# Kernel tuning notes

Hardware: AMD Instinct MI355X
Metric: run time of the kernel (lower is better)

The kernel has to match this reference:

```python
import jax, jax.numpy as jnp
import numpy as np

KSIZE = 21
SCALE = 4

def _conv1x1(h, w, b):
    # h: (B, Ci, H, W), w: (Co, Ci), b: (Co,)
    return jnp.einsum('oi,bihw->bohw', w, h) + b[None, :, None, None]

def setup_inputs() -> dict:
    key = jax.random.key(0)
    ks = jax.random.split(key, 8)
    B, C, H, W = 16, 3, 256, 256
    in_nc, nf, nb, K2 = 64, 64, 8, KSIZE * KSIZE
    Hl, Wl = H // SCALE, W // SCALE
    wscale = 0.1
    return {
        'x': jax.random.normal(ks[0], (B, C, H, W), jnp.float32),
        'z': jax.random.normal(ks[1], (B, in_nc, Hl, Wl), jnp.float32),
        'w_in': wscale * jax.random.normal(ks[2], (nf, in_nc), jnp.float32),
        'b_in': jnp.zeros((nf,), jnp.float32),
        'res_w1': wscale * jax.random.normal(ks[3], (nb, nf, nf), jnp.float32),
        'res_b1': jnp.zeros((nb, nf), jnp.float32),
        'res_w2': wscale * jax.random.normal(ks[4], (nb, nf, nf), jnp.float32),
        'res_b2': jnp.zeros((nb, nf), jnp.float32),
        'w_out': wscale * jax.random.normal(ks[5], (K2, nf), jnp.float32),
        'b_out': jnp.zeros((K2,), jnp.float32),
    }

def reference(x, z, w_in, b_in, res_w1, res_b1, res_w2, res_b2, w_out, b_out):
    B, C, H, W = x.shape
    Hl, Wl = z.shape[2], z.shape[3]
    K2 = KSIZE * KSIZE
    pad = KSIZE // 2

    # --- kernel prediction trunk (all 1x1 convs) ---
    h = _conv1x1(z, w_in, b_in)
    for i in range(res_w1.shape[0]):  # fixed n_layers loop
        r = _conv1x1(h, res_w1[i], res_b1[i])
        r = _conv1x1(jax.nn.relu(r), res_w2[i], res_b2[i])
        h = h + r
    logits = _conv1x1(h, w_out, b_out)            # (B, K2, Hl, Wl)
    kernel = jax.nn.softmax(logits, axis=1)       # softmax over kernel taps

    # --- reflection pad + unfold (im2col) with stride=scale ---
    xp = jnp.pad(x, ((0, 0), (0, 0), (pad, pad), (pad, pad)), mode='reflect')
    xr = xp.reshape(B * C, 1, H + 2 * pad, W + 2 * pad)
    patches = jax.lax.conv_general_dilated_patches(
        xr, filter_shape=(KSIZE, KSIZE), window_strides=(SCALE, SCALE),
        padding='VALID', dimension_numbers=('NCHW', 'OIHW', 'NCHW'))
    patches = patches.reshape(B, C, K2, Hl, Wl)   # (B, C, K2, Hl, Wl)

    # --- per-pixel spatially-varying kernel apply ---
    out = (patches * kernel[:, None]).sum(axis=2)  # (B, C, Hl, Wl)
    return out, kernel
```

## Files before the change

### kernel.cpp

```cpp
#include <hip/hip_runtime.h>
#include <math.h>

#define KS 21
#define K2 441
#define NB 8
#define PPI 4096
#define NPIX 65536
#define STR 72
#define XW 276
#define BPX 128
#define NTH 512
#define XROWS 25

typedef unsigned short u16;
typedef unsigned int u32;
typedef short short8v __attribute__((ext_vector_type(8)));
typedef float f32x4 __attribute__((ext_vector_type(4)));
typedef float f32x16 __attribute__((ext_vector_type(16)));

#define WOUT_OFF 69632
#define BOUT_BYTE 196608

#define LDS_HBUF  0
#define LDS_XS    18432
#define LDS_SBUF  59840
#define LDS_OBUF  60864
#define LDS_TOTAL 63936

__device__ __forceinline__ u16 f2bf(float x)
{
    union { float f; u32 u; } c; c.f = x;
    u32 r = c.u + 0x7FFF + ((c.u >> 16) & 1);
    return (u16)(r >> 16);
}
__device__ __forceinline__ float bflo(u32 w)
{ union { u32 u; float f; } c; c.u = w << 16; return c.f; }
__device__ __forceinline__ float bfhi(u32 w)
{ union { u32 u; float f; } c; c.u = w & 0xffff0000u; return c.f; }
__device__ __forceinline__ float u16f(u16 h)
{ union { u32 u; float f; } c; c.u = ((u32)h) << 16; return c.f; }

__device__ __forceinline__ int xcd_swz(int i)
{
    return ((i & 7) << 6) | (i >> 3);
}

__global__ void prep_kernel(const float* __restrict__ w_in,
                            const float* __restrict__ rw1,
                            const float* __restrict__ rw2,
                            const float* __restrict__ w_out,
                            const float* __restrict__ b_out,
                            u16* __restrict__ wsu, float* __restrict__ bout)
{
    int idx = blockIdx.x * 256 + threadIdx.x;
    if (idx < 69632) {
        int u = idx & 4095;
        int j = u & 7, lane = (u >> 3) & 63, frag = (u >> 9) & 7;
        int kk = frag >> 2, nt = frag & 3, layer = idx >> 12;
        int i = kk * 32 + (lane >> 4) * 8 + j;
        int o = nt * 16 + (lane & 15);
        const float* src;
        if (layer == 0) src = w_in;
        else if (layer & 1) src = rw1 + ((layer - 1) >> 1) * 4096;
        else src = rw2 + ((layer - 2) >> 1) * 4096;
        wsu[idx] = f2bf(src[o * 64 + i]);
    } else if (idx < 69632 + 28672) {
        int u = idx - 69632;
        int j = u & 7, lane = (u >> 3) & 63, t6 = u >> 9;
        int t = t6 % 14, kk = t6 / 14;
        int tap = t * 32 + (lane & 31);
        int i = kk * 16 + (lane >> 5) * 8 + j;
        wsu[idx] = f2bf((tap < K2) ? w_out[tap * 64 + i] : 0.f);
    } else if (idx < 69632 + 28672 + 448) {
        int tap = idx - (69632 + 28672);
        bout[tap] = (tap < K2) ? b_out[tap] : -100.f;
    }
}

__device__ __forceinline__ int reflect256(int v)
{
    v = (v < 0) ? -v : v;
    return (v > 255) ? (510 - v) : v;
}

template <int MODE>
__device__ __forceinline__ void do_layer(u16* hb, const u16* __restrict__ wb,
                                         const float* __restrict__ bias,
                                         float* hreg, int aoff, int wbase,
                                         int c, int g, int lane)
{
    short8v a0 = *(const short8v*)(hb + aoff);
    short8v a1 = *(const short8v*)(hb + aoff + 32);
#pragma unroll
    for (int nt = 0; nt < 4; ++nt) {
        f32x4 acc = {};
        short8v b0 = *(const short8v*)(wb + ((nt)     * 64 + lane) * 8);
        short8v b1 = *(const short8v*)(wb + ((4 + nt) * 64 + lane) * 8);
        acc = __builtin_amdgcn_mfma_f32_16x16x32_bf16(a0, b0, acc, 0, 0, 0);
        acc = __builtin_amdgcn_mfma_f32_16x16x32_bf16(a1, b1, acc, 0, 0, 0);
        const float bv = bias[nt * 16 + c];
#pragma unroll
        for (int r = 0; r < 4; ++r) {
            float v = acc[r] + bv;
            if (MODE == 1) v = fmaxf(v, 0.f);
            if (MODE == 2) { v += hreg[nt * 4 + r]; hreg[nt * 4 + r] = v; }
            if (MODE == 0) hreg[nt * 4 + r] = v;
            hb[(wbase + g * 4 + r) * STR + nt * 16 + c] = f2bf(v);
        }
    }
}

__launch_bounds__(NTH, 4)
__global__ void trunk_kernel(const float* __restrict__ z,
                             const float* __restrict__ x,
                             const float* __restrict__ b_in,
                             const float* __restrict__ rb1,
                             const float* __restrict__ rb2,
                             const u16* __restrict__ wsu,
                             const float* __restrict__ bout,
                             float* __restrict__ out,
                             float* __restrict__ kout)
{
    extern __shared__ __align__(16) char smem[];
    u16*   hbuf = (u16*)(smem + LDS_HBUF);
    u16*   xs   = (u16*)(smem + LDS_XS);
    float* sbuf = (float*)(smem + LDS_SBUF);
    float* obuf = (float*)(smem + LDS_OBUF);

    const int tid = threadIdx.x, lane = tid & 63, wave = tid >> 6;
    const int pix0 = xcd_swz(blockIdx.x) * BPX;
    const int b = pix0 >> 12, rem0 = pix0 & 4095;
    const int hl0 = rem0 >> 6;

    {
        const int p = tid & 127, i0 = (tid >> 7) * 16;
        const float* zp = z + ((size_t)b * 64 + i0) * PPI + rem0 + p;
        u32* dst = (u32*)hbuf + p * (STR / 2) + i0 / 2;
#pragma unroll
        for (int i = 0; i < 16; i += 2) {
            float v0 = zp[(size_t)i * PPI];
            float v1 = zp[(size_t)(i + 1) * PPI];
            dst[i / 2] = (u32)f2bf(v0) | ((u32)f2bf(v1) << 16);
        }
    }
    for (int u = tid; u < XROWS * 3 * XW; u += NTH) {
        int t = u / XW;
        int j = u - t * XW;
        int rr = t / 3, cch = t - rr * 3;
        int row = reflect256(hl0 * 4 + rr - 10);
        int xcol = reflect256(j - 10);
        xs[u] = f2bf(x[(((size_t)b * 3 + cch) * 256 + row) * 256 + xcol]);
    }
    __syncthreads();

    const int c16 = lane & 15, g4 = lane >> 4;
    const int wbase = wave * 16;
    const int aoff = (wbase + c16) * STR + g4 * 8;
    float hreg[16];

    do_layer<0>(hbuf, wsu, b_in, hreg, aoff, wbase, c16, g4, lane);
#pragma unroll 1
    for (int l = 0; l < NB; ++l) {
        do_layer<1>(hbuf, wsu + (size_t)(1 + 2 * l) * 4096, rb1 + l * 64,
                    hreg, aoff, wbase, c16, g4, lane);
        do_layer<2>(hbuf, wsu + (size_t)(2 + 2 * l) * 4096, rb2 + l * 64,
                    hreg, aoff, wbase, c16, g4, lane);
    }
    __syncthreads();

    const int c32 = lane & 31, hi2 = lane >> 5;
    const int wavepx = (wave >> 1) * 32;
    const int tbase = (wave & 1) * 7;

    short8v bh[4];
#pragma unroll
    for (int kk = 0; kk < 4; ++kk)
        bh[kk] = *(const short8v*)(hbuf + (wavepx + c32) * STR + kk * 16 + hi2 * 8);

    float ssum = 0.f;
    u32 epack[56];
    const u16* wob = wsu + WOUT_OFF;
#pragma unroll
    for (int ti = 0; ti < 7; ++ti) {
        const int t = tbase + ti;
        f32x16 acc = {};
#pragma unroll
        for (int kk = 0; kk < 4; ++kk) {
            short8v aw = *(const short8v*)(wob + ((kk * 14 + t) * 64 + lane) * 8);
            acc = __builtin_amdgcn_mfma_f32_32x32x16_bf16(aw, bh[kk], acc, 0, 0, 0);
        }
#pragma unroll
        for (int rr = 0; rr < 8; ++rr) {
            const int r0 = 2 * rr;
            const int tap0 = t * 32 + (r0 & 3) + 8 * (r0 >> 2) + 4 * hi2;
            float e0 = __expf(acc[r0] + bout[tap0]);
            float e1 = __expf(acc[r0 + 1] + bout[tap0 + 1]);
            ssum += e0 + e1;
            epack[ti * 8 + rr] = (u32)f2bf(e0) | ((u32)f2bf(e1) << 16);
        }
    }
    ssum += __shfl_xor(ssum, 32);
    if (lane < 32) sbuf[wave * 32 + lane] = ssum;
    __syncthreads();
    const float inv_s = 1.f / (ssum + sbuf[(wave ^ 1) * 32 + c32]);

    const int pxl = wavepx + c32;
    const int wl = pxl & 63, hlr = pxl >> 6;
    const int xcb = wl * 4;
    float* kbase = kout + (size_t)b * K2 * PPI + rem0 + pxl;
    float oacc0 = 0.f, oacc1 = 0.f, oacc2 = 0.f;

#pragma unroll
    for (int ti = 0; ti < 7; ++ti) {
        const int t = tbase + ti;
        int tap = t * 32 + 4 * hi2;
        int ky = tap / KS;
        int kx = tap - ky * KS;
#pragma unroll
        for (int rr = 0; rr < 8; ++rr) {
            const u32 ep = epack[ti * 8 + rr];
            float p0 = bflo(ep) * inv_s;
            float p1 = bfhi(ep) * inv_s;
            if (tap < K2) {
                kbase[(size_t)tap * PPI] = p0;
                const u16* xp = xs + ((hlr * 4 + ky) * 3) * XW + xcb + kx;
                oacc0 = fmaf(p0, u16f(xp[0]), oacc0);
                oacc1 = fmaf(p0, u16f(xp[XW]), oacc1);
                oacc2 = fmaf(p0, u16f(xp[2 * XW]), oacc2);
            }
            tap += 1; kx += 1; if (kx >= KS) { kx -= KS; ky += 1; }
            if (tap < K2) {
                kbase[(size_t)tap * PPI] = p1;
                const u16* xp = xs + ((hlr * 4 + ky) * 3) * XW + xcb + kx;
                oacc0 = fmaf(p1, u16f(xp[0]), oacc0);
                oacc1 = fmaf(p1, u16f(xp[XW]), oacc1);
                oacc2 = fmaf(p1, u16f(xp[2 * XW]), oacc2);
            }
            const int d = (rr & 1) ? 5 : 1;
            tap += d; kx += d; if (kx >= KS) { kx -= KS; ky += 1; }
        }
    }

    oacc0 += __shfl_xor(oacc0, 32);
    oacc1 += __shfl_xor(oacc1, 32);
    oacc2 += __shfl_xor(oacc2, 32);
    if (lane < 32) {
        obuf[(wave * 3 + 0) * 32 + lane] = oacc0;
        obuf[(wave * 3 + 1) * 32 + lane] = oacc1;
        obuf[(wave * 3 + 2) * 32 + lane] = oacc2;
    }
    __syncthreads();
    if ((wave & 1) == 0 && lane < 32) {
        const int o = rem0 + wavepx + lane;
#pragma unroll
        for (int cch = 0; cch < 3; ++cch) {
            float v = obuf[(wave * 3 + cch) * 32 + lane] +
                      obuf[((wave + 1) * 3 + cch) * 32 + lane];
            out[((size_t)b * 3 + cch) * PPI + o] = v;
        }
    }
}

extern "C" void kernel_launch(void* const* d_in, const int* in_sizes, int n_in,
                              void* d_out, int out_size, void* d_ws, size_t ws_size,
                              hipStream_t stream)
{
    const float* x     = (const float*)d_in[0];
    const float* z     = (const float*)d_in[1];
    const float* w_in  = (const float*)d_in[2];
    const float* b_in  = (const float*)d_in[3];
    const float* rw1   = (const float*)d_in[4];
    const float* rb1   = (const float*)d_in[5];
    const float* rw2   = (const float*)d_in[6];
    const float* rb2   = (const float*)d_in[7];
    const float* w_out = (const float*)d_in[8];
    const float* b_out = (const float*)d_in[9];

    float* out  = (float*)d_out;
    float* kout = out + (size_t)16 * 3 * PPI;
    u16*   wsu  = (u16*)d_ws;
    float* bout = (float*)((char*)d_ws + BOUT_BYTE);

    (void)hipFuncSetAttribute((const void*)trunk_kernel,
                              hipFuncAttributeMaxDynamicSharedMemorySize,
                              LDS_TOTAL);

    prep_kernel<<<(69632 + 28672 + 448 + 255) / 256, 256, 0, stream>>>(
        w_in, rw1, rw2, w_out, b_out, wsu, bout);

    trunk_kernel<<<NPIX / BPX, NTH, LDS_TOTAL, stream>>>(
        z, x, b_in, rb1, rb2, wsu, bout, out, kout);
}
```

Baseline: 78.58 us.

## Recompute output-head MFMA instead of caching exps; remap waves to full 64-pixel rows

The 56-register epack array that held bf16 exp values between the softmax-sum pass and the apply pass is removed. The output-head MFMAs and exps are now recomputed in the second pass, so register pressure drops. Waves are regrouped so each handles two 32-pixel halves (one full 64-pixel row), and lanes are shuffled so every lane owns one pixel with coalesced 64-wide kernel stores. LDS shrinks because sbuf and obuf now reuse the hbuf region. The cost is double MFMA and exp work plus an extra barrier.

After: 89.23 us. +13.6%, slower.

```diff
diff --git a/kernel.cpp b/kernel.cpp
--- a/kernel.cpp
+++ b/kernel.cpp
@@ -23,9 +23,7 @@
 
 #define LDS_HBUF  0
 #define LDS_XS    18432
-#define LDS_SBUF  59840
-#define LDS_OBUF  60864
-#define LDS_TOTAL 63936
+#define LDS_TOTAL 59840
 
 __device__ __forceinline__ u16 f2bf(float x)
 {
@@ -33,10 +31,6 @@
     u32 r = c.u + 0x7FFF + ((c.u >> 16) & 1);
     return (u16)(r >> 16);
 }
-__device__ __forceinline__ float bflo(u32 w)
-{ union { u32 u; float f; } c; c.u = w << 16; return c.f; }
-__device__ __forceinline__ float bfhi(u32 w)
-{ union { u32 u; float f; } c; c.u = w & 0xffff0000u; return c.f; }
 __device__ __forceinline__ float u16f(u16 h)
 { union { u32 u; float f; } c; c.u = ((u32)h) << 16; return c.f; }
 
@@ -124,8 +118,8 @@
     extern __shared__ __align__(16) char smem[];
     u16*   hbuf = (u16*)(smem + LDS_HBUF);
     u16*   xs   = (u16*)(smem + LDS_XS);
-    float* sbuf = (float*)(smem + LDS_SBUF);
-    float* obuf = (float*)(smem + LDS_OBUF);
+    float* sbuf = (float*)(smem);
+    float* obuf = (float*)(smem + 2048);
 
     const int tid = threadIdx.x, lane = tid & 63, wave = tid >> 6;
     const int pix0 = xcd_swz(blockIdx.x) * BPX;
@@ -169,94 +163,149 @@
     __syncthreads();
 
     const int c32 = lane & 31, hi2 = lane >> 5;
-    const int wavepx = (wave >> 1) * 32;
-    const int tbase = (wave & 1) * 7;
-
-    short8v bh[4];
-#pragma unroll
-    for (int kk = 0; kk < 4; ++kk)
-        bh[kk] = *(const short8v*)(hbuf + (wavepx + c32) * STR + kk * 16 + hi2 * 8);
-
-    float ssum = 0.f;
-    u32 epack[56];
+    const int q   = wave >> 2;
+    const int s   = (wave >> 1) & 1;
+    const int par = wave & 1;
+    const int t0  = par * 7 + (s ? 4 : 0);
+    const int ntile = s ? 3 : 4;
+
+    short8v bhA[4], bhB[4];
+#pragma unroll
+    for (int kk = 0; kk < 4; ++kk) {
+        bhA[kk] = *(const short8v*)(hbuf + (64 * q + c32) * STR + kk * 16 + hi2 * 8);
+        bhB[kk] = *(const short8v*)(hbuf + (64 * q + 32 + c32) * STR + kk * 16 + hi2 * 8);
+    }
+    __syncthreads();
+
     const u16* wob = wsu + WOUT_OFF;
-#pragma unroll
-    for (int ti = 0; ti < 7; ++ti) {
-        const int t = tbase + ti;
-        f32x16 acc = {};
+
+    float ssA = 0.f, ssB = 0.f;
+#pragma unroll
+    for (int ti = 0; ti < 4; ++ti) if (ti < ntile) {
+        const int t = t0 + ti;
+        f32x16 accA = {}, accB = {};
 #pragma unroll
         for (int kk = 0; kk < 4; ++kk) {
             short8v aw = *(const short8v*)(wob + ((kk * 14 + t) * 64 + lane) * 8);
-            acc = __builtin_amdgcn_mfma_f32_32x32x16_bf16(aw, bh[kk], acc, 0, 0, 0);
+            accA = __builtin_amdgcn_mfma_f32_32x32x16_bf16(aw, bhA[kk], accA, 0, 0, 0);
+            accB = __builtin_amdgcn_mfma_f32_32x32x16_bf16(aw, bhB[kk], accB, 0, 0, 0);
         }
 #pragma unroll
         for (int rr = 0; rr < 8; ++rr) {
             const int r0 = 2 * rr;
             const int tap0 = t * 32 + (r0 & 3) + 8 * (r0 >> 2) + 4 * hi2;
-            float e0 = __expf(acc[r0] + bout[tap0]);
-            float e1 = __expf(acc[r0 + 1] + bout[tap0 + 1]);
-            ssum += e0 + e1;
-            epack[ti * 8 + rr] = (u32)f2bf(e0) | ((u32)f2bf(e1) << 16);
-        }
-    }
-    ssum += __shfl_xor(ssum, 32);
-    if (lane < 32) sbuf[wave * 32 + lane] = ssum;
-    __syncthreads();
-    const float inv_s = 1.f / (ssum + sbuf[(wave ^ 1) * 32 + c32]);
-
-    const int pxl = wavepx + c32;
-    const int wl = pxl & 63, hlr = pxl >> 6;
-    const int xcb = wl * 4;
-    float* kbase = kout + (size_t)b * K2 * PPI + rem0 + pxl;
+            ssA += __expf(accA[r0] + bout[tap0]) + __expf(accA[r0 + 1] + bout[tap0 + 1]);
+            ssB += __expf(accB[r0] + bout[tap0]) + __expf(accB[r0 + 1] + bout[tap0 + 1]);
+        }
+    }
+    ssA += __shfl_xor(ssA, 32);
+    ssB += __shfl_xor(ssB, 32);
+    if (lane < 32) sbuf[(wave * 2 + 0) * 32 + lane] = ssA;
+    else           sbuf[(wave * 2 + 1) * 32 + (lane & 31)] = ssB;
+    __syncthreads();
+    float ssum = 0.f;
+#pragma unroll
+    for (int j = 0; j < 4; ++j)
+        ssum += sbuf[((4 * q + j) * 2 + hi2) * 32 + c32];
+    const float inv_s = 1.f / ssum;
+
+    float* kb = kout + (size_t)b * K2 * PPI + rem0 + 64 * q + lane;
     float oacc0 = 0.f, oacc1 = 0.f, oacc2 = 0.f;
-
-#pragma unroll
-    for (int ti = 0; ti < 7; ++ti) {
-        const int t = tbase + ti;
-        int tap = t * 32 + 4 * hi2;
-        int ky = tap / KS;
-        int kx = tap - ky * KS;
+    const int xrb = 4 * q;
+    const u16* xcb = xs + lane * 4;
+
+#pragma unroll
+    for (int ti = 0; ti < 4; ++ti) if (ti < ntile) {
+        const int t = t0 + ti;
+        f32x16 accA = {}, accB = {};
+#pragma unroll
+        for (int kk = 0; kk < 4; ++kk) {
+            short8v aw = *(const short8v*)(wob + ((kk * 14 + t) * 64 + lane) * 8);
+            accA = __builtin_amdgcn_mfma_f32_32x32x16_bf16(aw, bhA[kk], accA, 0, 0, 0);
+            accB = __builtin_amdgcn_mfma_f32_32x32x16_bf16(aw, bhB[kk], accB, 0, 0, 0);
+        }
+        int tapb = t * 32;
+        int ky0 = tapb / KS, kx0 = tapb - ky0 * KS;
 #pragma unroll
         for (int rr = 0; rr < 8; ++rr) {
-            const u32 ep = epack[ti * 8 + rr];
-            float p0 = bflo(ep) * inv_s;
-            float p1 = bfhi(ep) * inv_s;
-            if (tap < K2) {
-                kbase[(size_t)tap * PPI] = p0;
-                const u16* xp = xs + ((hlr * 4 + ky) * 3) * XW + xcb + kx;
-                oacc0 = fmaf(p0, u16f(xp[0]), oacc0);
-                oacc1 = fmaf(p0, u16f(xp[XW]), oacc1);
-                oacc2 = fmaf(p0, u16f(xp[2 * XW]), oacc2);
+            const int r0 = 2 * rr;
+            const int tap0 = tapb + 4 * hi2;
+            const float eA0 = __expf(accA[r0] + bout[tap0]);
+            const float eA1 = __expf(accA[r0 + 1] + bout[tap0 + 1]);
+            const float eB0 = __expf(accB[r0] + bout[tap0]);
+            const float eB1 = __expf(accB[r0 + 1] + bout[tap0 + 1]);
+            const float a0s = __shfl_xor(eA0, 32), b0s = __shfl_xor(eB0, 32);
+            const float a1s = __shfl_xor(eA1, 32), b1s = __shfl_xor(eB1, 32);
+            const bool lo = (lane < 32);
+            const float pv0 = (lo ? eA0 : b0s) * inv_s;
+            const float pv1 = (lo ? eA1 : b1s) * inv_s;
+            const float pv4 = (lo ? a0s : eB0) * inv_s;
+            const float pv5 = (lo ? a1s : eB1) * inv_s;
+            {
+                const int T = tapb;
+                if (T < K2) {
+                    kb[(size_t)T * PPI] = pv0;
+                    const u16* xp = xcb + ((xrb + ky0) * 3) * XW + kx0;
+                    oacc0 = fmaf(pv0, u16f(xp[0]), oacc0);
+                    oacc1 = fmaf(pv0, u16f(xp[XW]), oacc1);
+                    oacc2 = fmaf(pv0, u16f(xp[2 * XW]), oacc2);
+                }
             }
-            tap += 1; kx += 1; if (kx >= KS) { kx -= KS; ky += 1; }
-            if (tap < K2) {
-                kbase[(size_t)tap * PPI] = p1;
-                const u16* xp = xs + ((hlr * 4 + ky) * 3) * XW + xcb + kx;
-                oacc0 = fmaf(p1, u16f(xp[0]), oacc0);
-                oacc1 = fmaf(p1, u16f(xp[XW]), oacc1);
-                oacc2 = fmaf(p1, u16f(xp[2 * XW]), oacc2);
+            {
+                const int T = tapb + 1;
+                if (T < K2) {
+                    int kx = kx0 + 1, ky = ky0;
+                    if (kx >= KS) { kx -= KS; ++ky; }
+                    kb[(size_t)T * PPI] = pv1;
+                    const u16* xp = xcb + ((xrb + ky) * 3) * XW + kx;
+                    oacc0 = fmaf(pv1, u16f(xp[0]), oacc0);
+                    oacc1 = fmaf(pv1, u16f(xp[XW]), oacc1);
+                    oacc2 = fmaf(pv1, u16f(xp[2 * XW]), oacc2);
+                }
             }
-            const int d = (rr & 1) ? 5 : 1;
-            tap += d; kx += d; if (kx >= KS) { kx -= KS; ky += 1; }
-        }
-    }
-
-    oacc0 += __shfl_xor(oacc0, 32);
-    oacc1 += __shfl_xor(oacc1, 32);
-    oacc2 += __shfl_xor(oacc2, 32);
-    if (lane < 32) {
-        obuf[(wave * 3 + 0) * 32 + lane] = oacc0;
-        obuf[(wave * 3 + 1) * 32 + lane] = oacc1;
-        obuf[(wave * 3 + 2) * 32 + lane] = oacc2;
-    }
-    __syncthreads();
-    if ((wave & 1) == 0 && lane < 32) {
-        const int o = rem0 + wavepx + lane;
+            {
+                const int T = tapb + 4;
+                if (T < K2) {
+                    int kx = kx0 + 4, ky = ky0;
+                    if (kx >= KS) { kx -= KS; ++ky; }
+                    kb[(size_t)T * PPI] = pv4;
+                    const u16* xp = xcb + ((xrb + ky) * 3) * XW + kx;
+                    oacc0 = fmaf(pv4, u16f(xp[0]), oacc0);
+                    oacc1 = fmaf(pv4, u16f(xp[XW]), oacc1);
+                    oacc2 = fmaf(pv4, u16f(xp[2 * XW]), oacc2);
+                }
+            }
+            {
+                const int T = tapb + 5;
+                if (T < K2) {
+                    int kx = kx0 + 5, ky = ky0;
+                    if (kx >= KS) { kx -= KS; ++ky; }
+                    kb[(size_t)T * PPI] = pv5;
+                    const u16* xp = xcb + ((xrb + ky) * 3) * XW + kx;
+                    oacc0 = fmaf(pv5, u16f(xp[0]), oacc0);
+                    oacc1 = fmaf(pv5, u16f(xp[XW]), oacc1);
+                    oacc2 = fmaf(pv5, u16f(xp[2 * XW]), oacc2);
+                }
+            }
+            const int st = (rr & 1) ? 6 : 2;
+            tapb += st; kx0 += st;
+            if (kx0 >= KS) { kx0 -= KS; ++ky0; }
+        }
+    }
+
+    obuf[(wave * 3 + 0) * 64 + lane] = oacc0;
+    obuf[(wave * 3 + 1) * 64 + lane] = oacc1;
+    obuf[(wave * 3 + 2) * 64 + lane] = oacc2;
+    __syncthreads();
+    if (tid < BPX) {
+        const int qq = tid >> 6, o = tid & 63;
 #pragma unroll
         for (int cch = 0; cch < 3; ++cch) {
-            float v = obuf[(wave * 3 + cch) * 32 + lane] +
-                      obuf[((wave + 1) * 3 + cch) * 32 + lane];
-            out[((size_t)b * 3 + cch) * PPI + o] = v;
+            float v = 0.f;
+#pragma unroll
+            for (int j = 0; j < 4; ++j)
+                v += obuf[((4 * qq + j) * 3 + cch) * 64 + o];
+            out[((size_t)b * 3 + cch) * PPI + rem0 + tid] = v;
         }
     }
 }
```

## Double block size and stage softmax kernel output through LDS for coalesced stores

Applied to the files above, without the earlier changes.

Each block now covers 256 pixels with 1024 threads instead of 128 with 512, and the x tile grows to 33 rows. The kernel-probability output is no longer written per lane as scattered scalar stores. It goes into an LDS transpose buffer as bf16 and is then written to global memory as 16-byte vector stores per tap row. This targets the uncoalesced kout write traffic. In exchange it adds per-iteration barriers, lowers occupancy to one large block, and rounds the stored kernel values to bf16, which loses precision.

New measurement: 86.29 us. +9.8%, slower.

```diff
diff --git a/kernel.cpp b/kernel.cpp
--- a/kernel.cpp
+++ b/kernel.cpp
@@ -8,9 +8,9 @@
 #define NPIX 65536
 #define STR 72
 #define XW 276
-#define BPX 128
-#define NTH 512
-#define XROWS 25
+#define BPX 256
+#define NTH 1024
+#define XROWS 33
 
 typedef unsigned short u16;
 typedef unsigned int u32;
@@ -21,11 +21,9 @@
 #define WOUT_OFF 69632
 #define BOUT_BYTE 196608
 
-#define LDS_HBUF  0
-#define LDS_XS    18432
-#define LDS_SBUF  59840
-#define LDS_OBUF  60864
-#define LDS_TOTAL 63936
+#define LDS_XS    36864
+#define LDS_TOTAL 91520
+#define PB_STRIDE 260
 
 __device__ __forceinline__ u16 f2bf(float x)
 {
@@ -42,7 +40,7 @@
 
 __device__ __forceinline__ int xcd_swz(int i)
 {
-    return ((i & 7) << 6) | (i >> 3);
+    return ((i & 7) << 5) | (i >> 3);
 }
 
 __global__ void prep_kernel(const float* __restrict__ w_in,
@@ -110,7 +108,7 @@
     }
 }
 
-__launch_bounds__(NTH, 4)
+__launch_bounds__(NTH, 1)
 __global__ void trunk_kernel(const float* __restrict__ z,
                              const float* __restrict__ x,
                              const float* __restrict__ b_in,
@@ -122,10 +120,11 @@
                              float* __restrict__ kout)
 {
     extern __shared__ __align__(16) char smem[];
-    u16*   hbuf = (u16*)(smem + LDS_HBUF);
+    u16*   hbuf = (u16*)(smem);
     u16*   xs   = (u16*)(smem + LDS_XS);
-    float* sbuf = (float*)(smem + LDS_SBUF);
-    float* obuf = (float*)(smem + LDS_OBUF);
+    u16*   pbuf = (u16*)(smem);
+    float* sbuf = (float*)(smem + 33280);
+    float* obuf = (float*)(smem);
 
     const int tid = threadIdx.x, lane = tid & 63, wave = tid >> 6;
     const int pix0 = xcd_swz(blockIdx.x) * BPX;
@@ -133,7 +132,7 @@
     const int hl0 = rem0 >> 6;
 
     {
-        const int p = tid & 127, i0 = (tid >> 7) * 16;
+        const int p = tid & 255, i0 = (tid >> 8) * 16;
         const float* zp = z + ((size_t)b * 64 + i0) * PPI + rem0 + p;
         u32* dst = (u32*)hbuf + p * (STR / 2) + i0 / 2;
 #pragma unroll
@@ -170,12 +169,14 @@
 
     const int c32 = lane & 31, hi2 = lane >> 5;
     const int wavepx = (wave >> 1) * 32;
-    const int tbase = (wave & 1) * 7;
+    const int par = wave & 1;
+    const int tbase = par * 7;
 
     short8v bh[4];
 #pragma unroll
     for (int kk = 0; kk < 4; ++kk)
         bh[kk] = *(const short8v*)(hbuf + (wavepx + c32) * STR + kk * 16 + hi2 * 8);
+    __syncthreads();
 
     float ssum = 0.f;
     u32 epack[56];
@@ -207,10 +208,11 @@
     const int pxl = wavepx + c32;
     const int wl = pxl & 63, hlr = pxl >> 6;
     const int xcb = wl * 4;
-    float* kbase = kout + (size_t)b * K2 * PPI + rem0 + pxl;
+    float* kb = kout + (size_t)b * K2 * PPI + rem0;
     float oacc0 = 0.f, oacc1 = 0.f, oacc2 = 0.f;
-
-#pragma unroll
+    const int rowbase = par * 32;
+
+#pragma unroll 1
     for (int ti = 0; ti < 7; ++ti) {
         const int t = tbase + ti;
         int tap = t * 32 + 4 * hi2;
@@ -221,24 +223,37 @@
             const u32 ep = epack[ti * 8 + rr];
             float p0 = bflo(ep) * inv_s;
             float p1 = bfhi(ep) * inv_s;
+            pbuf[(rowbase + (tap - t * 32)) * PB_STRIDE + pxl] = f2bf(p0);
             if (tap < K2) {
-                kbase[(size_t)tap * PPI] = p0;
                 const u16* xp = xs + ((hlr * 4 + ky) * 3) * XW + xcb + kx;
                 oacc0 = fmaf(p0, u16f(xp[0]), oacc0);
                 oacc1 = fmaf(p0, u16f(xp[XW]), oacc1);
                 oacc2 = fmaf(p0, u16f(xp[2 * XW]), oacc2);
             }
-            tap += 1; kx += 1; if (kx >= KS) { kx -= KS; ky += 1; }
+            tap += 1; kx += 1; if (kx >= KS) { kx -= KS; ++ky; }
+            pbuf[(rowbase + (tap - t * 32)) * PB_STRIDE + pxl] = f2bf(p1);
             if (tap < K2) {
-                kbase[(size_t)tap * PPI] = p1;
                 const u16* xp = xs + ((hlr * 4 + ky) * 3) * XW + xcb + kx;
                 oacc0 = fmaf(p1, u16f(xp[0]), oacc0);
                 oacc1 = fmaf(p1, u16f(xp[XW]), oacc1);
                 oacc2 = fmaf(p1, u16f(xp[2 * XW]), oacc2);
             }
             const int d = (rr & 1) ? 5 : 1;
-            tap += d; kx += d; if (kx >= KS) { kx -= KS; ky += 1; }
-        }
+            tap += d; kx += d; if (kx >= KS) { kx -= KS; ++ky; }
+        }
+        __syncthreads();
+#pragma unroll
+        for (int j = 0; j < 4; ++j) {
+            const int row = wave * 4 + j;
+            const int T = ((row >> 5) * 7 + ti) * 32 + (row & 31);
+            if (T < K2) {
+                const u32* pr = (const u32*)(pbuf + row * PB_STRIDE) + lane * 2;
+                const u32 w0 = pr[0], w1 = pr[1];
+                f32x4 o4 = { bflo(w0), bfhi(w0), bflo(w1), bfhi(w1) };
+                *(f32x4*)(kb + (size_t)T * PPI + 4 * lane) = o4;
+            }
+        }
+        __syncthreads();
     }
 
     oacc0 += __shfl_xor(oacc0, 32);
```
